# Performance work log

Hardware: AMD Instinct MI355X
Metric: run time of the kernel (lower is better)

The kernel has to match this reference:

```python
import jax, jax.numpy as jnp
import numpy as np

N, F, T, H, E = 50000, 8, 12, 64, 1600000

def _glorot(k, shape):
    lim = float(np.sqrt(6.0 / (shape[0] + shape[1])))
    return jax.random.uniform(k, shape, jnp.float32, -lim, lim)

def setup_inputs() -> dict:
    key = jax.random.key(0)
    ks = jax.random.split(key, 12)
    return {
        "x": jax.random.normal(ks[0], (N, F, T), jnp.float32),
        "edge_index": jax.random.randint(ks[1], (2, E), 0, N, jnp.int32),
        "edge_attr": jax.random.uniform(ks[2], (E,), jnp.float32),
        # GCNConv weights (conv_z/r/h): in_channels=F -> out_channels=H, plus bias
        "Wz": _glorot(ks[3], (F, H)), "bz": jnp.zeros((H,), jnp.float32),
        "Wr": _glorot(ks[4], (F, H)), "br": jnp.zeros((H,), jnp.float32),
        "Wh": _glorot(ks[5], (F, H)), "bh": jnp.zeros((H,), jnp.float32),
        # GRU linears: Linear(2H -> H)
        "Wlz": _glorot(ks[6], (2 * H, H)), "blz": jnp.zeros((H,), jnp.float32),
        "Wlr": _glorot(ks[7], (2 * H, H)), "blr": jnp.zeros((H,), jnp.float32),
        "Wlh": _glorot(ks[8], (2 * H, H)), "blh": jnp.zeros((H,), jnp.float32),
        # A3TGCN attention over periods
        "att": jax.random.uniform(ks[9], (T,), jnp.float32),
        # output head: Linear(H -> periods)
        "Wout": _glorot(ks[10], (H, T)), "bout": jnp.zeros((T,), jnp.float32),
    }

def _gcn_norm(edge_index, edge_attr, n):
    # GCNConv: add self-loops (weight 1), symmetric D^-1/2 (A+I) D^-1/2 normalization
    loop = jnp.arange(n, dtype=edge_index.dtype)
    src = jnp.concatenate([edge_index[0], loop])
    dst = jnp.concatenate([edge_index[1], loop])
    ew = jnp.concatenate([edge_attr, jnp.ones((n,), edge_attr.dtype)])
    deg = jax.ops.segment_sum(ew, dst, num_segments=n)
    dinv = jnp.where(deg > 0, jax.lax.rsqrt(deg), 0.0)
    return src, dst, dinv[src] * ew * dinv[dst]

def reference(x, edge_index, edge_attr, Wz, bz, Wr, br, Wh, bh,
              Wlz, blz, Wlr, blr, Wlh, blh, att, Wout, bout):
    n, _, periods = x.shape
    hid = Wz.shape[1]
    src, dst, nw = _gcn_norm(edge_index, edge_attr, n)

    def conv(xw, b):  # xw: [n, hid] features already multiplied by conv weight
        return jax.ops.segment_sum(nw[:, None] * xw[src], dst, num_segments=n) + b

    probs = jax.nn.softmax(att)
    # Upstream A3TGCN passes the SAME initial hidden (None -> zeros) to every period
    H0 = jnp.zeros((n, hid), x.dtype)
    acc = jnp.zeros((n, hid), x.dtype)
    for t in range(periods):
        xt = x[:, :, t]  # [n, F]
        Z = jax.nn.sigmoid(jnp.concatenate([conv(xt @ Wz, bz), H0], axis=1) @ Wlz + blz)
        R = jax.nn.sigmoid(jnp.concatenate([conv(xt @ Wr, br), H0], axis=1) @ Wlr + blr)
        Ht = jnp.tanh(jnp.concatenate([conv(xt @ Wh, bh), H0 * R], axis=1) @ Wlh + blh)
        acc = acc + probs[t] * (Z * H0 + (1.0 - Z) * Ht)
    h = jax.nn.relu(acc)
    return h @ Wout + bout
```

## Files before the change

### kernel.cpp

```cpp
#include <hip/hip_runtime.h>


#define NN 50000
#define EE 1600000
#define FT 96
#define TP 12
#define FF 8
#define HH 64
#define CAP 128
#define NPART 196

__global__ void __launch_bounds__(256) k_init(int* counts) {
    int n = blockIdx.x * 256 + threadIdx.x;
    if (n < NN) counts[n] = 0;
}

__global__ void __launch_bounds__(256) k_build(const int* ei, const float* ea,
                                               int* counts, int2* csrf) {
    int e = blockIdx.x * 256 + threadIdx.x;
    if (e < EE) {
        int d = ei[EE + e];
        int slot = atomicAdd(&counts[d], 1);
        if (slot < CAP)
            csrf[(size_t)d * CAP + slot] = make_int2(ei[e], __float_as_int(ea[e]));
    }
}

__global__ void __launch_bounds__(256) k_degxs(const float* __restrict__ x,
                                               const int* __restrict__ counts,
                                               const int2* __restrict__ csrf,
                                               float* __restrict__ dinv,
                                               float* __restrict__ xs) {
    int wave = threadIdx.x >> 6;
    int lane = threadIdx.x & 63;
    int n = blockIdx.x * 4 + wave;
    if (n >= NN) return;
    int cnt = min(counts[n], CAP);
    int jb = n * CAP, je = jb + cnt;
    float s = 0.0f;
    for (int j = jb + lane; j < je; j += 64) s += __int_as_float(csrf[j].y);
    for (int off = 32; off > 0; off >>= 1) s += __shfl_xor(s, off, 64);
    float di = rsqrtf(1.0f + s);
    if (lane == 0) dinv[n] = di;
    if (lane < 24) {
        float4 v = ((const float4*)(x + (size_t)n * FT))[lane];
        ((float4*)(xs + (size_t)n * FT))[lane] =
            make_float4(di * v.x, di * v.y, di * v.z, di * v.w);
    }
}

__global__ void __launch_bounds__(64) k_fold(const float* Wz, const float* bz,
                                             const float* Wh, const float* bh,
                                             const float* Wlz, const float* blz,
                                             const float* Wlh, const float* blh,
                                             const float* att, float* fold) {
    int h = threadIdx.x;
    for (int f = 0; f < FF; f++) {
        float sz = 0.0f, sh = 0.0f;
        for (int k = 0; k < HH; k++) {
            sz += Wz[f * HH + k] * Wlz[k * HH + h];
            sh += Wh[f * HH + k] * Wlh[k * HH + h];
        }
        fold[f * HH + h]       = sz;
        fold[512 + f * HH + h] = sh;
    }
    float cz = blz[h], ch = blh[h];
    for (int k = 0; k < HH; k++) {
        cz += bz[k] * Wlz[k * HH + h];
        ch += bh[k] * Wlh[k * HH + h];
    }
    fold[1024 + h] = cz;
    fold[1088 + h] = ch;
    if (h < TP) {
        float m = -1e30f;
        for (int t = 0; t < TP; t++) m = fmaxf(m, att[t]);
        float s = 0.0f;
        for (int t = 0; t < TP; t++) s += __expf(att[t] - m);
        fold[1152 + h] = __expf(att[h] - m) / s;
    }
}

__global__ void __launch_bounds__(256) k_aggmain(const float* __restrict__ xs,
                                                 const float* __restrict__ dinv,
                                                 const int* __restrict__ counts,
                                                 const int2* __restrict__ csrf,
                                                 const float* __restrict__ fold,
                                                 const float* __restrict__ Wout,
                                                 const float* __restrict__ bout,
                                                 float* __restrict__ out) {
    __shared__ float sMz[512], sMh[512], sczb[64], schb[64], sprobs[16], sWout[768], sbout[16];
    __shared__ float sy[4][FT];
    for (int i = threadIdx.x; i < 512; i += 256) { sMz[i] = fold[i]; sMh[i] = fold[512 + i]; }
    if (threadIdx.x < 64) {
        sczb[threadIdx.x] = fold[1024 + threadIdx.x];
        schb[threadIdx.x] = fold[1088 + threadIdx.x];
    }
    if (threadIdx.x < TP) {
        sprobs[threadIdx.x] = fold[1152 + threadIdx.x];
        sbout[threadIdx.x]  = bout[threadIdx.x];
    }
    for (int i = threadIdx.x; i < 768; i += 256) sWout[i] = Wout[i];

    int wave = threadIdx.x >> 6;
    int lane = threadIdx.x & 63;
    int n = blockIdx.x * 4 + wave;

    bool act = lane < 24;
    float ax = 0.0f, ay = 0.0f, az = 0.0f, aw = 0.0f;
    if (act) {
        float4 v = ((const float4*)(xs + (size_t)n * FT))[lane];
        ax = v.x; ay = v.y; az = v.z; aw = v.w;
    }
    int cnt = min(counts[n], CAP);
    int jb = __builtin_amdgcn_readfirstlane(n * CAP);
    int je = __builtin_amdgcn_readfirstlane(n * CAP + cnt);
    int j = jb;
    for (; j + 4 <= je; j += 4) {
        int2 m0 = csrf[j];
        int2 m1 = csrf[j + 1];
        int2 m2 = csrf[j + 2];
        int2 m3 = csrf[j + 3];
        if (act) {
            float4 v0 = ((const float4*)(xs + (size_t)m0.x * FT))[lane];
            float4 v1 = ((const float4*)(xs + (size_t)m1.x * FT))[lane];
            float4 v2 = ((const float4*)(xs + (size_t)m2.x * FT))[lane];
            float4 v3 = ((const float4*)(xs + (size_t)m3.x * FT))[lane];
            float w0_ = __int_as_float(m0.y);
            float w1_ = __int_as_float(m1.y);
            float w2_ = __int_as_float(m2.y);
            float w3_ = __int_as_float(m3.y);
            ax = fmaf(w0_, v0.x, ax); ay = fmaf(w0_, v0.y, ay);
            az = fmaf(w0_, v0.z, az); aw = fmaf(w0_, v0.w, aw);
            ax = fmaf(w1_, v1.x, ax); ay = fmaf(w1_, v1.y, ay);
            az = fmaf(w1_, v1.z, az); aw = fmaf(w1_, v1.w, aw);
            ax = fmaf(w2_, v2.x, ax); ay = fmaf(w2_, v2.y, ay);
            az = fmaf(w2_, v2.z, az); aw = fmaf(w2_, v2.w, aw);
            ax = fmaf(w3_, v3.x, ax); ay = fmaf(w3_, v3.y, ay);
            az = fmaf(w3_, v3.z, az); aw = fmaf(w3_, v3.w, aw);
        }
    }
    for (; j < je; j++) {
        int2 m = csrf[j];
        if (act) {
            float4 v = ((const float4*)(xs + (size_t)m.x * FT))[lane];
            float wgt = __int_as_float(m.y);
            ax = fmaf(wgt, v.x, ax); ay = fmaf(wgt, v.y, ay);
            az = fmaf(wgt, v.z, az); aw = fmaf(wgt, v.w, aw);
        }
    }
    if (act) {
        float di = dinv[n];
        ((float4*)sy[wave])[lane] = make_float4(di * ax, di * ay, di * az, di * aw);
    }
    __syncthreads();

    const float* y = sy[wave];
    int h = lane;
    float zp[TP], hp[TP];
    float cz = sczb[h], ch = schb[h];
    #pragma unroll
    for (int t = 0; t < TP; t++) { zp[t] = cz; hp[t] = ch; }
    #pragma unroll
    for (int f = 0; f < FF; f++) {
        float mz = sMz[f * HH + h], mh = sMh[f * HH + h];
        #pragma unroll
        for (int t = 0; t < TP; t++) {
            float yv = y[f * TP + t];
            zp[t] = fmaf(yv, mz, zp[t]);
            hp[t] = fmaf(yv, mh, hp[t]);
        }
    }
    float acc = 0.0f;
    #pragma unroll
    for (int t = 0; t < TP; t++) {
        float z = 1.0f / (1.0f + __expf(-zp[t]));
        float hv = fmaxf(hp[t], -30.0f);
        float e = __expf(-2.0f * hv);
        float th = (1.0f - e) / (1.0f + e);
        acc += sprobs[t] * (1.0f - z) * th;
    }
    float r = fmaxf(acc, 0.0f);

    float o[TP];
    #pragma unroll
    for (int jj = 0; jj < TP; jj++) o[jj] = r * sWout[h * TP + jj];
    #pragma unroll
    for (int m = 1; m < 64; m <<= 1) {
        #pragma unroll
        for (int jj = 0; jj < TP; jj++) o[jj] += __shfl_xor(o[jj], m, 64);
    }
    if (lane == 0) {
        float* op = out + (size_t)n * TP;
        #pragma unroll
        for (int jj = 0; jj < TP; jj++) op[jj] = o[jj] + sbout[jj];
    }
}

extern "C" void kernel_launch(void* const* d_in, const int* in_sizes, int n_in,
                              void* d_out, int out_size, void* d_ws, size_t ws_size,
                              hipStream_t stream) {
    const float* x    = (const float*)d_in[0];
    const int*   ei   = (const int*)d_in[1];
    const float* ea   = (const float*)d_in[2];
    const float* Wz   = (const float*)d_in[3];
    const float* bz   = (const float*)d_in[4];
    const float* Wh   = (const float*)d_in[7];
    const float* bh   = (const float*)d_in[8];
    const float* Wlz  = (const float*)d_in[9];
    const float* blz  = (const float*)d_in[10];
    const float* Wlh  = (const float*)d_in[13];
    const float* blh  = (const float*)d_in[14];
    const float* att  = (const float*)d_in[15];
    const float* Wout = (const float*)d_in[16];
    const float* bout = (const float*)d_in[17];
    float* out = (float*)d_out;

    char* w = (char*)d_ws;
    auto alloc = [&](size_t bytes) {
        char* p = w;
        w += (bytes + 255) & ~(size_t)255;
        return p;
    };
    int*   counts = (int*)alloc(NN * 4);
    int2*  csrf   = (int2*)alloc((size_t)NN * CAP * 8);
    float* dinv   = (float*)alloc(NN * 4);
    float* xs     = (float*)alloc((size_t)NN * FT * 4);
    float* fold   = (float*)alloc(2048 * 4);
    if ((size_t)(w - (char*)d_ws) > ws_size) return;

    hipLaunchKernelGGL(k_init,    dim3(NPART), dim3(256), 0, stream, counts);
    hipLaunchKernelGGL(k_build,   dim3((EE + 255) / 256), dim3(256), 0, stream, ei, ea, counts, csrf);
    hipLaunchKernelGGL(k_degxs,   dim3((NN + 3) / 4), dim3(256), 0, stream, x, counts, csrf, dinv, xs);
    hipLaunchKernelGGL(k_fold,    dim3(1), dim3(64), 0, stream, Wz, bz, Wh, bh, Wlz, blz, Wlh, blh, att, fold);
    hipLaunchKernelGGL(k_aggmain, dim3(NN / 4), dim3(256), 0, stream,
                       xs, dinv, counts, csrf, fold, Wout, bout, out);
}
```

Measured before the change: 265.9 us.

## Build CSR with shared-memory range binning and store gathered features in fp16

Replaces the global-atomic CSR build and its count-clear kernel with a single kernel where each block owns a range of 512 destination nodes and one of four edge chunks. Each block scans its whole chunk and counts per node with shared-memory atomics into fixed 32-slot sub-buckets, so there are no global atomics and no separate init launch. The pre-scaled node features used in the neighbor gather are now stored as fp16, halving the gather bytes. In exchange, every block rereads its full edge chunk (about 98x redundant reads of the destination array), each node keeps at most 32 edges per chunk, and fp16 storage loses precision.

```diff
diff --git a/kernel.cpp b/kernel.cpp
--- a/kernel.cpp
+++ b/kernel.cpp
@@ -1,4 +1,5 @@
 #include <hip/hip_runtime.h>
+#include <hip/hip_fp16.h>
 
 
 #define NN 50000
@@ -7,45 +8,69 @@
 #define TP 12
 #define FF 8
 #define HH 64
+#define RB 512
+#define NCH 4
+#define CHE 400000
+#define CCAP 32
 #define CAP 128
-#define NPART 196
-
-__global__ void __launch_bounds__(256) k_init(int* counts) {
-    int n = blockIdx.x * 256 + threadIdx.x;
-    if (n < NN) counts[n] = 0;
-}
-
-__global__ void __launch_bounds__(256) k_build(const int* ei, const float* ea,
-                                               int* counts, int2* csrf) {
-    int e = blockIdx.x * 256 + threadIdx.x;
-    if (e < EE) {
-        int d = ei[EE + e];
-        int slot = atomicAdd(&counts[d], 1);
-        if (slot < CAP)
-            csrf[(size_t)d * CAP + slot] = make_int2(ei[e], __float_as_int(ea[e]));
+#define NRANGE 98
+
+union Cv { ushort4 u; __half2 h[2]; };
+
+__global__ void __launch_bounds__(256) k_build2(const int* __restrict__ ei,
+                                                const float* __restrict__ ea,
+                                                int* __restrict__ counts2,
+                                                int2* __restrict__ csrf) {
+    int r = blockIdx.x / NCH;
+    int c = blockIdx.x % NCH;
+    int base = r * RB;
+    __shared__ int lcnt[RB];
+    for (int i = threadIdx.x; i < RB; i += 256) lcnt[i] = 0;
+    __syncthreads();
+    const int* dst = ei + EE;
+    int ebeg = c * CHE, eend = ebeg + CHE;
+    for (int e = ebeg + threadIdx.x; e < eend; e += 256) {
+        int d = dst[e];
+        unsigned rel = (unsigned)(d - base);
+        if (rel < RB) {
+            int slot = atomicAdd(&lcnt[rel], 1);
+            if (slot < CCAP)
+                csrf[(size_t)d * CAP + c * CCAP + slot] =
+                    make_int2(ei[e], __float_as_int(ea[e]));
+        }
+    }
+    __syncthreads();
+    for (int i = threadIdx.x; i < RB; i += 256) {
+        int n = base + i;
+        if (n < NN) counts2[c * NN + n] = min(lcnt[i], CCAP);
     }
 }
 
 __global__ void __launch_bounds__(256) k_degxs(const float* __restrict__ x,
-                                               const int* __restrict__ counts,
+                                               const int* __restrict__ counts2,
                                                const int2* __restrict__ csrf,
                                                float* __restrict__ dinv,
-                                               float* __restrict__ xs) {
+                                               __half* __restrict__ xsh) {
     int wave = threadIdx.x >> 6;
     int lane = threadIdx.x & 63;
     int n = blockIdx.x * 4 + wave;
     if (n >= NN) return;
-    int cnt = min(counts[n], CAP);
-    int jb = n * CAP, je = jb + cnt;
     float s = 0.0f;
-    for (int j = jb + lane; j < je; j += 64) s += __int_as_float(csrf[j].y);
+    #pragma unroll
+    for (int c = 0; c < NCH; c++) {
+        int cnt = counts2[c * NN + n];
+        if (lane < cnt)
+            s += __int_as_float(csrf[(size_t)n * CAP + c * CCAP + lane].y);
+    }
     for (int off = 32; off > 0; off >>= 1) s += __shfl_xor(s, off, 64);
     float di = rsqrtf(1.0f + s);
     if (lane == 0) dinv[n] = di;
     if (lane < 24) {
         float4 v = ((const float4*)(x + (size_t)n * FT))[lane];
-        ((float4*)(xs + (size_t)n * FT))[lane] =
-            make_float4(di * v.x, di * v.y, di * v.z, di * v.w);
+        Cv cc;
+        cc.h[0] = __floats2half2_rn(di * v.x, di * v.y);
+        cc.h[1] = __floats2half2_rn(di * v.z, di * v.w);
+        ((ushort4*)xsh)[(size_t)n * 24 + lane] = cc.u;
     }
 }
 
@@ -80,9 +105,9 @@
     }
 }
 
-__global__ void __launch_bounds__(256) k_aggmain(const float* __restrict__ xs,
+__global__ void __launch_bounds__(256) k_aggmain(const __half* __restrict__ xsh,
                                                  const float* __restrict__ dinv,
-                                                 const int* __restrict__ counts,
+                                                 const int* __restrict__ counts2,
                                                  const int2* __restrict__ csrf,
                                                  const float* __restrict__ fold,
                                                  const float* __restrict__ Wout,
@@ -105,47 +130,61 @@
     int lane = threadIdx.x & 63;
     int n = blockIdx.x * 4 + wave;
 
+    const ushort4* xsr = (const ushort4*)xsh;
+
     bool act = lane < 24;
     float ax = 0.0f, ay = 0.0f, az = 0.0f, aw = 0.0f;
     if (act) {
-        float4 v = ((const float4*)(xs + (size_t)n * FT))[lane];
-        ax = v.x; ay = v.y; az = v.z; aw = v.w;
-    }
-    int cnt = min(counts[n], CAP);
-    int jb = __builtin_amdgcn_readfirstlane(n * CAP);
-    int je = __builtin_amdgcn_readfirstlane(n * CAP + cnt);
-    int j = jb;
-    for (; j + 4 <= je; j += 4) {
-        int2 m0 = csrf[j];
-        int2 m1 = csrf[j + 1];
-        int2 m2 = csrf[j + 2];
-        int2 m3 = csrf[j + 3];
-        if (act) {
-            float4 v0 = ((const float4*)(xs + (size_t)m0.x * FT))[lane];
-            float4 v1 = ((const float4*)(xs + (size_t)m1.x * FT))[lane];
-            float4 v2 = ((const float4*)(xs + (size_t)m2.x * FT))[lane];
-            float4 v3 = ((const float4*)(xs + (size_t)m3.x * FT))[lane];
-            float w0_ = __int_as_float(m0.y);
-            float w1_ = __int_as_float(m1.y);
-            float w2_ = __int_as_float(m2.y);
-            float w3_ = __int_as_float(m3.y);
-            ax = fmaf(w0_, v0.x, ax); ay = fmaf(w0_, v0.y, ay);
-            az = fmaf(w0_, v0.z, az); aw = fmaf(w0_, v0.w, aw);
-            ax = fmaf(w1_, v1.x, ax); ay = fmaf(w1_, v1.y, ay);
-            az = fmaf(w1_, v1.z, az); aw = fmaf(w1_, v1.w, aw);
-            ax = fmaf(w2_, v2.x, ax); ay = fmaf(w2_, v2.y, ay);
-            az = fmaf(w2_, v2.z, az); aw = fmaf(w2_, v2.w, aw);
-            ax = fmaf(w3_, v3.x, ax); ay = fmaf(w3_, v3.y, ay);
-            az = fmaf(w3_, v3.z, az); aw = fmaf(w3_, v3.w, aw);
-        }
-    }
-    for (; j < je; j++) {
-        int2 m = csrf[j];
-        if (act) {
-            float4 v = ((const float4*)(xs + (size_t)m.x * FT))[lane];
-            float wgt = __int_as_float(m.y);
-            ax = fmaf(wgt, v.x, ax); ay = fmaf(wgt, v.y, ay);
-            az = fmaf(wgt, v.z, az); aw = fmaf(wgt, v.w, aw);
+        Cv c; c.u = xsr[(size_t)n * 24 + lane];
+        float2 a = __half22float2(c.h[0]);
+        float2 b = __half22float2(c.h[1]);
+        ax = a.x; ay = a.y; az = b.x; aw = b.y;
+    }
+    #pragma unroll
+    for (int ch = 0; ch < NCH; ch++) {
+        int cnt = __builtin_amdgcn_readfirstlane(counts2[ch * NN + n]);
+        int jb = __builtin_amdgcn_readfirstlane(n * CAP + ch * CCAP);
+        int je = jb + cnt;
+        int j = jb;
+        for (; j + 4 <= je; j += 4) {
+            int2 m0 = csrf[j];
+            int2 m1 = csrf[j + 1];
+            int2 m2 = csrf[j + 2];
+            int2 m3 = csrf[j + 3];
+            if (act) {
+                Cv c0, c1, c2, c3;
+                c0.u = xsr[(size_t)m0.x * 24 + lane];
+                c1.u = xsr[(size_t)m1.x * 24 + lane];
+                c2.u = xsr[(size_t)m2.x * 24 + lane];
+                c3.u = xsr[(size_t)m3.x * 24 + lane];
+                float w0_ = __int_as_float(m0.y);
+                float w1_ = __int_as_float(m1.y);
+                float w2_ = __int_as_float(m2.y);
+                float w3_ = __int_as_float(m3.y);
+                float2 a0 = __half22float2(c0.h[0]), b0 = __half22float2(c0.h[1]);
+                float2 a1 = __half22float2(c1.h[0]), b1 = __half22float2(c1.h[1]);
+                float2 a2 = __half22float2(c2.h[0]), b2 = __half22float2(c2.h[1]);
+                float2 a3 = __half22float2(c3.h[0]), b3 = __half22float2(c3.h[1]);
+                ax = fmaf(w0_, a0.x, ax); ay = fmaf(w0_, a0.y, ay);
+                az = fmaf(w0_, b0.x, az); aw = fmaf(w0_, b0.y, aw);
+                ax = fmaf(w1_, a1.x, ax); ay = fmaf(w1_, a1.y, ay);
+                az = fmaf(w1_, b1.x, az); aw = fmaf(w1_, b1.y, aw);
+                ax = fmaf(w2_, a2.x, ax); ay = fmaf(w2_, a2.y, ay);
+                az = fmaf(w2_, b2.x, az); aw = fmaf(w2_, b2.y, aw);
+                ax = fmaf(w3_, a3.x, ax); ay = fmaf(w3_, a3.y, ay);
+                az = fmaf(w3_, b3.x, az); aw = fmaf(w3_, b3.y, aw);
+            }
+        }
+        for (; j < je; j++) {
+            int2 m = csrf[j];
+            if (act) {
+                Cv c; c.u = xsr[(size_t)m.x * 24 + lane];
+                float wgt = __int_as_float(m.y);
+                float2 a = __half22float2(c.h[0]);
+                float2 b = __half22float2(c.h[1]);
+                ax = fmaf(wgt, a.x, ax); ay = fmaf(wgt, a.y, ay);
+                az = fmaf(wgt, b.x, az); aw = fmaf(wgt, b.y, aw);
+            }
         }
     }
     if (act) {
@@ -157,9 +196,9 @@
     const float* y = sy[wave];
     int h = lane;
     float zp[TP], hp[TP];
-    float cz = sczb[h], ch = schb[h];
-    #pragma unroll
-    for (int t = 0; t < TP; t++) { zp[t] = cz; hp[t] = ch; }
+    float cz = sczb[h], chb = schb[h];
+    #pragma unroll
+    for (int t = 0; t < TP; t++) { zp[t] = cz; hp[t] = chb; }
     #pragma unroll
     for (int f = 0; f < FF; f++) {
         float mz = sMz[f * HH + h], mh = sMh[f * HH + h];
@@ -221,17 +260,16 @@
         w += (bytes + 255) & ~(size_t)255;
         return p;
     };
-    int*   counts = (int*)alloc(NN * 4);
-    int2*  csrf   = (int2*)alloc((size_t)NN * CAP * 8);
-    float* dinv   = (float*)alloc(NN * 4);
-    float* xs     = (float*)alloc((size_t)NN * FT * 4);
-    float* fold   = (float*)alloc(2048 * 4);
+    int*    counts2 = (int*)alloc((size_t)NCH * NN * 4);
+    int2*   csrf    = (int2*)alloc((size_t)NN * CAP * 8);
+    float*  dinv    = (float*)alloc(NN * 4);
+    __half* xsh     = (__half*)alloc((size_t)NN * FT * 2);
+    float*  fold    = (float*)alloc(2048 * 4);
     if ((size_t)(w - (char*)d_ws) > ws_size) return;
 
-    hipLaunchKernelGGL(k_init,    dim3(NPART), dim3(256), 0, stream, counts);
-    hipLaunchKernelGGL(k_build,   dim3((EE + 255) / 256), dim3(256), 0, stream, ei, ea, counts, csrf);
-    hipLaunchKernelGGL(k_degxs,   dim3((NN + 3) / 4), dim3(256), 0, stream, x, counts, csrf, dinv, xs);
+    hipLaunchKernelGGL(k_build2,  dim3(NRANGE * NCH), dim3(256), 0, stream, ei, ea, counts2, csrf);
+    hipLaunchKernelGGL(k_degxs,   dim3((NN + 3) / 4), dim3(256), 0, stream, x, counts2, csrf, dinv, xsh);
     hipLaunchKernelGGL(k_fold,    dim3(1), dim3(64), 0, stream, Wz, bz, Wh, bh, Wlz, blz, Wlh, blh, att, fold);
     hipLaunchKernelGGL(k_aggmain, dim3(NN / 4), dim3(256), 0, stream,
-                       xs, dinv, counts, csrf, fold, Wout, bout, out);
-}
+                       xsh, dinv, counts2, csrf, fold, Wout, bout, out);
+}
```

Result: slower. 637.2 us (+139.6%).
